# Performance work log

Measured on AMD Instinct MI355X. Metric: run time of the kernel, lower is better.

The kernel has to match this reference:

```python
import jax, jax.numpy as jnp
import numpy as np

B, C_IN, N, K, UP = 4, 128, 1024, 9, 4
EPS_BN = 1e-5


def _grid():
    # gen_grid(4): num_x=num_y=2, linspace(-0.2,0.2,2) -> (4,2)
    g = jnp.linspace(-0.2, 0.2, 2)
    x, y = jnp.meshgrid(g, g, indexing='ij')
    return jnp.stack([x, y], axis=-1).reshape(-1, 2)


def _knn(x, k, dilation):
    # x: (B,C,N). L2-normalize features, matrix pairwise dist, top-k, dilated select.
    nrm = jnp.sqrt(jnp.sum(x * x, axis=1, keepdims=True))
    xn = x / jnp.maximum(nrm, 1e-12)
    xt = xn.transpose(0, 2, 1)                      # (B,N,C)
    sq = jnp.sum(xt * xt, axis=-1)                  # (B,N)
    dist = sq[:, :, None] - 2.0 * jnp.einsum('bnc,bmc->bnm', xt, xt) + sq[:, None, :]
    _, idx = jax.lax.top_k(-dist, k * dilation)     # k*d nearest (incl. self)
    return idx[:, :, ::dilation]                    # (B,N,k)


def _bn(x, g, b, axes):
    # training-mode batchnorm over given axes, channel axis = 1
    m = jnp.mean(x, axis=axes, keepdims=True)
    v = jnp.mean((x - m) ** 2, axis=axes, keepdims=True)
    sh = [1] * x.ndim
    sh[1] = -1
    return (x - m) * jax.lax.rsqrt(v + EPS_BN) * g.reshape(sh) + b.reshape(sh)


def _edge_conv(x, k, dil, W, g, b):
    # DGCNN edge conv: gather neighbors, [x_i, x_j-x_i], 1x1 conv, BN, relu, max over k
    idx = _knn(x, k, dil)                                        # (B,N,k)
    x_j = jax.vmap(lambda xx, ii: xx[:, ii])(x, idx)             # (B,C,N,k)
    x_i = jnp.broadcast_to(x[..., None], x_j.shape)
    feat = jnp.concatenate([x_i, x_j - x_i], axis=1)             # (B,2C,N,k)
    out = jnp.einsum('oc,bcnk->bonk', W, feat)
    out = jax.nn.relu(_bn(out, g, b, (0, 2, 3)))
    return jnp.max(out, axis=-1)                                 # (B,Cout,N)


def _conv1d(x, W, b):
    return jnp.einsum('oc,bcn->bon', W, x) + b[None, :, None]


def _atten(x, Wf, bf, gf, bef, Wg, bg, gg, beg, Wh, bh, gh, beh, gamma):
    # attention_unit / RA_Layer1 math (C=130)
    f = jax.nn.relu(_bn(_conv1d(x, Wf, bf), gf, bef, (0, 2)))    # (B,C/4,M)
    g_ = jax.nn.relu(_bn(_conv1d(x, Wg, bg), gg, beg, (0, 2)))
    h = jax.nn.relu(_bn(_conv1d(x, Wh, bh), gh, beh, (0, 2)))    # (B,C,M)
    s = jnp.einsum('bcn,bcm->bnm', g_, f)                        # g^T @ f: (B,M,M)
    beta = jax.nn.softmax(s, axis=2)
    o = jnp.einsum('bcn,bnm->bcm', h, beta)                      # h @ beta
    return gamma * o + x


def _forward(inp, Wa, gna, bta, Wb, gnb, btb, Wf, bf, gf, bef, Wg, bg, gg, beg,
             Wh, bh, gh, beh, gamma, W1, b1, W2, b2):
    x1 = _edge_conv(inp, K, 1, Wa, gna, bta)                     # (B,256,N)
    x2 = _edge_conv(inp, K, 2, Wb, gnb, btb)                     # (B,256,N)
    x = jnp.concatenate([x1, x2], axis=1)                        # (B,512,N)
    net = x.transpose(0, 2, 1).reshape(B, N * UP, 128)           # (B,4N,128)
    grid = jnp.repeat(_grid(), N, axis=0)                        # (4N,2)
    grid = jnp.broadcast_to(grid[None], (B, N * UP, 2)).astype(net.dtype)
    net = jnp.concatenate([net, grid], axis=2).transpose(0, 2, 1)  # (B,130,4N)
    net = _atten(net, Wf, bf, gf, bef, Wg, bg, gg, beg, Wh, bh, gh, beh, gamma)
    net = jax.nn.relu(_conv1d(net, W1, b1))                      # 130->256
    net = jax.nn.relu(_conv1d(net, W2, b2))                      # 256->128
    return net                                                   # (B,128,4N)


def setup_inputs() -> dict:
    key = jax.random.key(0)
    ks = jax.random.split(key, 24)
    rn = lambda k, sh, s=0.05: jax.random.normal(k, sh, jnp.float32) * s
    d = {
        'inp': jax.random.normal(ks[0], (B, C_IN, N), jnp.float32),
        'Wa': rn(ks[1], (256, 256)), 'gna': 1.0 + rn(ks[2], (256,)), 'bta': rn(ks[3], (256,)),
        'Wb': rn(ks[4], (256, 256)), 'gnb': 1.0 + rn(ks[5], (256,)), 'btb': rn(ks[6], (256,)),
        'Wf': rn(ks[7], (32, 130)), 'bf': rn(ks[8], (32,)), 'gf': 1.0 + rn(ks[9], (32,)), 'bef': rn(ks[9], (32,)),
        'Wg': rn(ks[10], (32, 130)), 'bg': rn(ks[11], (32,)), 'gg': 1.0 + rn(ks[12], (32,)), 'beg': rn(ks[12], (32,)),
        'Wh': rn(ks[13], (130, 130)), 'bh': rn(ks[14], (130,)), 'gh': 1.0 + rn(ks[15], (130,)), 'beh': rn(ks[15], (130,)),
        'gamma': rn(ks[16], (), 1.0),
        'W1': rn(ks[17], (256, 130)), 'b1': rn(ks[18], (256,)),
        'W2': rn(ks[19], (128, 256)), 'b2': rn(ks[20], (128,)),
    }
    return d


def reference(inp, Wa, gna, bta, Wb, gnb, btb, Wf, bf, gf, bef, Wg, bg, gg, beg,
              Wh, bh, gh, beh, gamma, W1, b1, W2, b2):
    return _forward(inp, Wa, gna, bta, Wb, gnb, btb, Wf, bf, gf, bef, Wg, bg, gg, beg,
                    Wh, bh, gh, beh, gamma, W1, b1, W2, b2)
```

## Files before the change

### kernel.cpp

```cpp
#include <hip/hip_runtime.h>

namespace {
constexpr int NB = 4;
constexpr int CI = 128;
constexpr int NP = 1024;
constexpr int MM = 4096;
constexpr float EPSBN = 1e-5f;
constexpr float LOG2E = 1.4426950408889634f;

constexpr size_t OPS_SH = 2162688;
constexpr size_t OFF_OP   = 0;
constexpr size_t OFF_DIST = 0;
constexpr size_t OFF_PM   = 0;
constexpr size_t OFF_QM   = 2097152;
constexpr size_t OFF_HRAW = 0;
constexpr size_t OFF_FGRAW= 2359296;
constexpr size_t OFF_Y1   = 0;
constexpr size_t OFF_FGT  = 6488064;
constexpr size_t OFF_HB   = 7012352;
constexpr size_t OFF_A16  = 6488064;
constexpr size_t OFF_X16  = 8192000;
constexpr size_t OFF_LSE  = 9502720;
constexpr size_t OFF_LSEP = 9519104;
constexpr size_t OFF_STATS= 9650176;
constexpr size_t OFF_ABE  = 9715712;
constexpr size_t OFF_ABFG = 9716736;
constexpr size_t OFF_ABH  = 9716864;
constexpr size_t OFF_FGP  = 9717376;
constexpr size_t OFF_BIAS = 9725568;
constexpr size_t OFF_W16  = 9726208;
constexpr size_t OFF_KNN  = 9779712;
constexpr size_t OFF_XN   = 9853440;
constexpr size_t OFF_SQ   = 10377728;
constexpr size_t OFF_XR   = 10381824;
constexpr size_t OFF_WPQ  = 10643968;
constexpr size_t W16_FG = 0;
constexpr size_t W16_H  = 10240;
constexpr size_t W16_C1 = 33280;
constexpr size_t W16_C2 = 74240;
constexpr size_t B_FG = 0, B_H = 64, B_C1 = 208, B_C2 = 464;
}

typedef __attribute__((ext_vector_type(8))) short short8;
typedef __attribute__((ext_vector_type(4))) float f32x4;
#define MFMA16(A, B, C) __builtin_amdgcn_mfma_f32_16x16x32_bf16(A, B, C, 0, 0, 0)

__device__ inline unsigned short f2bf(float x) {
  unsigned int u = __float_as_uint(x);
  unsigned int r = u + 0x7fff + ((u >> 16) & 1);
  return (unsigned short)(r >> 16);
}
__device__ inline float bf2f(unsigned short s) {
  return __uint_as_float(((unsigned int)s) << 16);
}
__device__ inline unsigned cvtpk(float lo, float hi) {
  unsigned r;
  asm("v_cvt_pk_bf16_f32 %0, %1, %2" : "=v"(r) : "v"(lo), "v"(hi));
  return r;
}

__global__ __launch_bounds__(256) void k_prep(const float* __restrict__ Wf, const float* __restrict__ Wg,
                                              const float* __restrict__ Wh, const float* __restrict__ W1,
                                              const float* __restrict__ W2, const float* __restrict__ bf,
                                              const float* __restrict__ bg, const float* __restrict__ bh,
                                              const float* __restrict__ b1, const float* __restrict__ b2,
                                              unsigned short* __restrict__ W16, float* __restrict__ BIAS) {
  int i = blockIdx.x * 256 + threadIdx.x;
  if (i < 107008) {
    float v = 0.f;
    if (i < 10240) { int o = i / 160, c = i % 160; if (c < 130) v = (o < 32) ? Wf[o * 130 + c] : Wg[(o - 32) * 130 + c]; }
    else if (i < 33280) { int r = i - 10240; int o = r / 160, c = r % 160; if (o < 130 && c < 130) v = Wh[o * 130 + c]; }
    else if (i < 74240) { int r = i - 33280; int o = r / 160, c = r % 160; if (c < 130) v = W1[o * 130 + c]; }
    else { int r = i - 74240; int o = r / 256, c = r % 256; v = W2[o * 256 + c]; }
    W16[i] = f2bf(v);
  } else if (i < 107648) {
    int j = i - 107008; float v = 0.f;
    if (j < 64) v = (j < 32) ? bf[j] : bg[j - 32];
    else if (j < 208) { int c = j - 64; if (c < 130) v = bh[c]; }
    else if (j < 464) v = b1[j - 208];
    else if (j < 592) v = b2[j - 464];
    BIAS[j] = v;
  }
}

__global__ __launch_bounds__(256) void k_prep2(const float* __restrict__ Wa, const float* __restrict__ Wb,
                                               unsigned short* __restrict__ WPQ) {
  int i = blockIdx.x * 256 + threadIdx.x;
  int e = i >> 16;
  int rem = i & 65535;
  int pq = rem >> 15;
  int rr = rem & 32767;
  int o = rr >> 7, c = rr & 127;
  const float* W = e ? Wb : Wa;
  float w1 = W[o * 256 + c], w2 = W[o * 256 + 128 + c];
  float v = pq ? w2 : (w1 - w2);
  WPQ[i] = f2bf(v);
}

__global__ __launch_bounds__(256) void k_norm(const float* __restrict__ x,
                                              float* __restrict__ xn,
                                              unsigned short* __restrict__ XR,
                                              float* __restrict__ sq) {
  int t = blockIdx.x * 256 + threadIdx.x;
  int b = t >> 10, n = t & 1023;
  const float* xb = x + (size_t)b * CI * NP + n;
  float ss = 0.f;
  #pragma unroll 4
  for (int c = 0; c < CI; ++c) { float v = xb[(size_t)c * NP]; ss += v * v; }
  float inv = 1.f / fmaxf(sqrtf(ss), 1e-12f);
  float* xo = xn + (size_t)b * CI * NP + n;
  float s2 = 0.f;
  for (int c0 = 0; c0 < 128; c0 += 8) {
    unsigned rw[4];
    #pragma unroll
    for (int j = 0; j < 4; ++j) {
      float va = xb[(size_t)(c0 + 2 * j) * NP];
      float vb = xb[(size_t)(c0 + 2 * j + 1) * NP];
      float na = va * inv, nb = vb * inv;
      s2 += na * na + nb * nb;
      xo[(size_t)(c0 + 2 * j) * NP] = na;
      xo[(size_t)(c0 + 2 * j + 1) * NP] = nb;
      rw[j] = (unsigned)f2bf(va) | ((unsigned)f2bf(vb) << 16);
    }
    uint4 r4 = {rw[0], rw[1], rw[2], rw[3]};
    *(uint4*)&XR[(size_t)t * 128 + c0] = r4;
  }
  sq[t] = s2;
}

__global__ __launch_bounds__(256) void k_dist(const float* __restrict__ xn,
                                              const float* __restrict__ sq,
                                              float* __restrict__ dist) {
  __shared__ float As[32][68], Bs[32][68];
  int t = threadIdx.x;
  int m0 = blockIdx.x * 64, n0 = blockIdx.y * 64, b = blockIdx.z;
  int mg = t & 15, ng = t >> 4;
  float acc[16];
  #pragma unroll
  for (int i = 0; i < 16; ++i) acc[i] = 0.f;
  for (int cc = 0; cc < 128; cc += 32) {
    __syncthreads();
    for (int idx = t; idx < 2048; idx += 256) {
      int c = idx >> 6, j = idx & 63;
      As[c][j] = xn[((size_t)b * CI + cc + c) * NP + n0 + j];
      Bs[c][j] = xn[((size_t)b * CI + cc + c) * NP + m0 + j];
    }
    __syncthreads();
    #pragma unroll
    for (int c = 0; c < 32; ++c) {
      float4 avv = *(const float4*)&As[c][ng * 4];
      float4 bvv = *(const float4*)&Bs[c][mg * 4];
      float a[4] = {avv.x, avv.y, avv.z, avv.w};
      float bb[4] = {bvv.x, bvv.y, bvv.z, bvv.w};
      #pragma unroll
      for (int i = 0; i < 4; ++i)
        #pragma unroll
        for (int j = 0; j < 4; ++j) acc[i * 4 + j] += a[i] * bb[j];
    }
  }
  #pragma unroll
  for (int i = 0; i < 4; ++i) {
    int n = n0 + ng * 4 + i;
    float sn = sq[b * NP + n];
    float4 r;
    r.x = sn + sq[b * NP + m0 + mg * 4 + 0] - 2.f * acc[i * 4 + 0];
    r.y = sn + sq[b * NP + m0 + mg * 4 + 1] - 2.f * acc[i * 4 + 1];
    r.z = sn + sq[b * NP + m0 + mg * 4 + 2] - 2.f * acc[i * 4 + 2];
    r.w = sn + sq[b * NP + m0 + mg * 4 + 3] - 2.f * acc[i * 4 + 3];
    *(float4*)&dist[((size_t)b * NP + n) * NP + m0 + mg * 4] = r;
  }
}

__global__ __launch_bounds__(64) void k_knn(const float* __restrict__ dist,
                                            int* __restrict__ knn) {
  int row = blockIdx.x;
  int l = threadIdx.x;
  const float* dr = dist + (size_t)row * NP;
  float d[16];
  #pragma unroll
  for (int i = 0; i < 16; ++i) d[i] = dr[l + 64 * i];
  for (int s = 0; s < 18; ++s) {
    float best = __builtin_inff(); int bslot = -1;
    #pragma unroll
    for (int i = 0; i < 16; ++i) if (d[i] < best) { best = d[i]; bslot = i; }
    int bidx = (bslot >= 0) ? (l + 64 * bslot) : 0x7fffffff;
    float bd = best; int bi = bidx;
    #pragma unroll
    for (int off = 32; off > 0; off >>= 1) {
      float od = __shfl_xor(bd, off);
      int   oi = __shfl_xor(bi, off);
      if (od < bd || (od == bd && oi < bi)) { bd = od; bi = oi; }
    }
    if (l == 0) knn[row * 18 + s] = bi;
    if ((bi & 63) == l) d[bi >> 6] = __builtin_inff();
  }
}

__global__ __launch_bounds__(256) void k_pqm(const unsigned short* __restrict__ XR,
                                             const unsigned short* __restrict__ WPQ,
                                             float* __restrict__ Pm,
                                             float* __restrict__ Qm) {
  int t = threadIdx.x; int w = t >> 6; int l = t & 63;
  int lm = l & 15, g = l >> 4;
  int nt = blockIdx.x, oq = blockIdx.y, z = blockIdx.z;
  int e = z >> 2, b = z & 3;
  int srow = nt * 64 + w * 16 + lm;
  const unsigned short* sp = XR + ((size_t)b * 1024 + srow) * 128 + 8 * g;
  const unsigned short* wpp = WPQ + ((size_t)(e * 2 + 0) * 256 + oq * 64 + lm) * 128 + 8 * g;
  const unsigned short* wqq = WPQ + ((size_t)(e * 2 + 1) * 256 + oq * 64 + lm) * 128 + 8 * g;
  f32x4 accp[4], accq[4];
  #pragma unroll
  for (int i = 0; i < 4; ++i) { accp[i] = {0.f, 0.f, 0.f, 0.f}; accq[i] = {0.f, 0.f, 0.f, 0.f}; }
  #pragma unroll
  for (int cc = 0; cc < 4; ++cc) {
    short8 bfr = *(const short8*)(sp + cc * 32);
    #pragma unroll
    for (int ct = 0; ct < 4; ++ct) {
      short8 ap = *(const short8*)(wpp + (size_t)ct * 16 * 128 + cc * 32);
      accp[ct] = MFMA16(ap, bfr, accp[ct]);
      short8 aq = *(const short8*)(wqq + (size_t)ct * 16 * 128 + cc * 32);
      accq[ct] = MFMA16(aq, bfr, accq[ct]);
    }
  }
  int eb = e * 4 + b;
  #pragma unroll
  for (int ct = 0; ct < 4; ++ct) {
    int o0 = oq * 64 + ct * 16 + 4 * g;
    float4 rp = {accp[ct][0], accp[ct][1], accp[ct][2], accp[ct][3]};
    float4 rq = {accq[ct][0], accq[ct][1], accq[ct][2], accq[ct][3]};
    *(float4*)&Pm[((size_t)eb * 1024 + srow) * 256 + o0] = rp;
    *(float4*)&Qm[((size_t)eb * 1024 + srow) * 256 + o0] = rq;
  }
}

__global__ __launch_bounds__(256) void k_edge_stats(const float* __restrict__ Pm,
                                                    const float* __restrict__ Qm,
                                                    const int* __restrict__ knn,
                                                    float* __restrict__ stats) {
  int o = threadIdx.x;
  int chunk = blockIdx.x, b = blockIdx.y, e = blockIdx.z;
  int eb = e * 4 + b;
  float s = 0.f, s2 = 0.f;
  for (int nn = 0; nn < 64; ++nn) {
    int n = chunk * 64 + nn;
    float p = Pm[((size_t)eb * 1024 + n) * 256 + o];
    const int* kn = knn + (b * 1024 + n) * 18;
    #pragma unroll
    for (int kk = 0; kk < 9; ++kk) {
      int j = kn[e ? 2 * kk : kk];
      float v = p + Qm[((size_t)eb * 1024 + j) * 256 + o];
      s += v; s2 += v * v;
    }
  }
  size_t idx = ((((size_t)e * 4 + b) * 16 + chunk) * 256 + o) * 2;
  stats[idx] = s; stats[idx + 1] = s2;
}

__global__ __launch_bounds__(256) void k_edge_fin(const float* __restrict__ stats,
                                                  const float* __restrict__ gna, const float* __restrict__ bta,
                                                  const float* __restrict__ gnb, const float* __restrict__ btb,
                                                  float* __restrict__ ab) {
  int i = blockIdx.x * 256 + threadIdx.x;
  if (i >= 512) return;
  int e = i >> 8, o = i & 255;
  float s = 0.f, s2 = 0.f;
  for (int b = 0; b < 4; ++b)
    for (int ch = 0; ch < 16; ++ch) {
      size_t idx = ((((size_t)e * 4 + b) * 16 + ch) * 256 + o) * 2;
      s += stats[idx]; s2 += stats[idx + 1];
    }
  float cnt = 4.0f * 1024.0f * 9.0f;
  float mean = s / cnt;
  float var = s2 / cnt - mean * mean;
  float g = e ? gnb[o] : gna[o];
  float bt = e ? btb[o] : bta[o];
  float alpha = g * rsqrtf(var + EPSBN);
  ab[i * 2] = alpha; ab[i * 2 + 1] = bt - mean * alpha;
}

__global__ __launch_bounds__(256) void k_edge_apply(const float* __restrict__ Pm,
                                                    const float* __restrict__ Qm,
                                                    const int* __restrict__ knn,
                                                    const float* __restrict__ ab,
                                                    unsigned short* __restrict__ X16) {
  __shared__ int knl[18];
  int t = threadIdx.x;
  int n = blockIdx.x, b = blockIdx.y;
  if (t < 18) knl[t] = knn[(b * 1024 + n) * 18 + t];
  __syncthreads();
  int e = t >> 7, oo = t & 127;
  int eb = e * 4 + b;
  const float* Pr = Pm + ((size_t)eb * 1024 + n) * 256;
  const float* Qb = Qm + (size_t)eb * 1024 * 256;
  float p0 = Pr[oo], p1 = Pr[oo + 128];
  float a0 = ab[(e * 256 + oo) * 2], be0 = ab[(e * 256 + oo) * 2 + 1];
  float a1 = ab[(e * 256 + oo + 128) * 2], be1 = ab[(e * 256 + oo + 128) * 2 + 1];
  float mx0 = -__builtin_inff(), mx1 = -__builtin_inff();
  #pragma unroll
  for (int kk = 0; kk < 9; ++kk) {
    int j = knl[e ? 2 * kk : kk];
    const float* Qr = Qb + (size_t)j * 256;
    mx0 = fmaxf(mx0, fmaf(a0, p0 + Qr[oo], be0));
    mx1 = fmaxf(mx1, fmaf(a1, p1 + Qr[oo + 128], be1));
  }
  int u0 = e << 1, u1 = (e << 1) | 1;
  X16[((size_t)b * MM + 4 * n + u0) * 160 + oo] = f2bf(fmaxf(mx0, 0.f));
  X16[((size_t)b * MM + 4 * n + u1) * 160 + oo] = f2bf(fmaxf(mx1, 0.f));
  if (t < 128) {
    int u = t >> 5, c = 128 + (t & 31);
    int gr = n >> 8;
    float v = (c == 128) ? ((gr < 2) ? -0.2f : 0.2f) : (c == 129) ? ((gr & 1) ? 0.2f : -0.2f) : 0.f;
    X16[((size_t)b * MM + 4 * n + u) * 160 + c] = f2bf(v);
  }
}

template <int KSTEPS, int CTPER, int OUTMODE, bool RELU>
__global__ __launch_bounds__(256) void k_convm(const unsigned short* __restrict__ src,
                                               const unsigned short* __restrict__ W16,
                                               const float* __restrict__ bias,
                                               float* __restrict__ dstF,
                                               unsigned short* __restrict__ dstB,
                                               int outld, int rows) {
  constexpr int LD = KSTEPS * 32;
  int t = threadIdx.x; int w = t >> 6; int l = t & 63;
  int lm = l & 15, g = l >> 4;
  int b = blockIdx.z; int ct0 = blockIdx.y * CTPER;
  int srow = blockIdx.x * 64 + w * 16 + lm;
  const unsigned short* sp = src + ((size_t)b * MM + srow) * LD + 8 * g;
  const unsigned short* wp = W16 + ((size_t)ct0 * 16 + lm) * LD + 8 * g;
  f32x4 acc[CTPER];
  #pragma unroll
  for (int i = 0; i < CTPER; ++i) acc[i] = {0.f, 0.f, 0.f, 0.f};
  #pragma unroll
  for (int cc = 0; cc < KSTEPS; ++cc) {
    short8 bfr = *(const short8*)(sp + cc * 32);
    #pragma unroll
    for (int ct = 0; ct < CTPER; ++ct) {
      short8 af = *(const short8*)(wp + (size_t)ct * 16 * LD + cc * 32);
      acc[ct] = MFMA16(af, bfr, acc[ct]);
    }
  }
  #pragma unroll
  for (int ct = 0; ct < CTPER; ++ct) {
    int o0 = (ct0 + ct) * 16 + 4 * g;
    float4 bv = *(const float4*)&bias[o0];
    float v[4] = {acc[ct][0] + bv.x, acc[ct][1] + bv.y, acc[ct][2] + bv.z, acc[ct][3] + bv.w};
    if (RELU) { v[0] = fmaxf(v[0], 0.f); v[1] = fmaxf(v[1], 0.f); v[2] = fmaxf(v[2], 0.f); v[3] = fmaxf(v[3], 0.f); }
    if (OUTMODE == 0) {
      float4 r = {v[0], v[1], v[2], v[3]};
      *(float4*)&dstF[((size_t)b * MM + srow) * outld + o0] = r;
    } else if (OUTMODE == 1) {
      uint2 pk;
      pk.x = cvtpk(v[0], v[1]);
      pk.y = cvtpk(v[2], v[3]);
      *(uint2*)&dstB[((size_t)b * MM + srow) * outld + o0] = pk;
    } else {
      #pragma unroll
      for (int r = 0; r < 4; ++r)
        dstF[((size_t)b * rows + o0 + r) * MM + srow] = v[r];
    }
  }
}

__global__ __launch_bounds__(256) void k_fgstats(const float* __restrict__ FGraw,
                                                 float* __restrict__ FGP) {
  __shared__ float red[4][64][2];
  int t = threadIdx.x; int c = t & 63, rq = t >> 6;
  int blk = blockIdx.x;
  float s = 0.f, s2 = 0.f;
  for (int k = 0; k < 64; ++k) {
    int r = blk * 256 + rq + 4 * k;
    float v = FGraw[(size_t)r * 64 + c];
    s += v; s2 += v * v;
  }
  red[rq][c][0] = s; red[rq][c][1] = s2;
  __syncthreads();
  if (t < 64) {
    float a = 0.f, a2 = 0.f;
    #pragma unroll
    for (int q = 0; q < 4; ++q) { a += red[q][t][0]; a2 += red[q][t][1]; }
    FGP[((size_t)blk * 64 + t) * 2] = a; FGP[((size_t)blk * 64 + t) * 2 + 1] = a2;
  }
}

__global__ __launch_bounds__(64) void k_fgfin(const float* __restrict__ FGP,
                                              const float* __restrict__ gf, const float* __restrict__ bef,
                                              const float* __restrict__ gg, const float* __restrict__ beg,
                                              float* __restrict__ ab) {
  int c = threadIdx.x;
  float s = 0.f, s2 = 0.f;
  for (int blk = 0; blk < 64; ++blk) { s += FGP[((size_t)blk * 64 + c) * 2]; s2 += FGP[((size_t)blk * 64 + c) * 2 + 1]; }
  float cnt = 16384.f;
  float mean = s / cnt, var = s2 / cnt - mean * mean;
  float gv = (c < 32) ? gf[c] : gg[c - 32];
  float bv = (c < 32) ? bef[c] : beg[c - 32];
  float alpha = gv * rsqrtf(var + EPSBN);
  ab[c * 2] = alpha; ab[c * 2 + 1] = bv - mean * alpha;
}

__global__ __launch_bounds__(256) void k_bnstats(const float* __restrict__ src,
                                                 const float* __restrict__ g,
                                                 const float* __restrict__ be,
                                                 float* __restrict__ ab, int ldC) {
  int o = blockIdx.x;
  int t = threadIdx.x;
  float s = 0.f, s2 = 0.f;
  for (int b = 0; b < NB; ++b) {
    const float* r = src + ((size_t)b * ldC + o) * MM;
    for (int m = t; m < MM; m += 256) { float v = r[m]; s += v; s2 += v * v; }
  }
  __shared__ float rs[256], rs2[256];
  rs[t] = s; rs2[t] = s2;
  __syncthreads();
  for (int off = 128; off > 0; off >>= 1) {
    if (t < off) { rs[t] += rs[t + off]; rs2[t] += rs2[t + off]; }
    __syncthreads();
  }
  if (t == 0) {
    float cnt = 16384.0f;
    float mean = rs[0] / cnt, var = rs2[0] / cnt - mean * mean;
    float alpha = g[o] * rsqrtf(var + EPSBN);
    ab[o * 2] = alpha; ab[o * 2 + 1] = be[o] - mean * alpha;
  }
}

__global__ __launch_bounds__(256) void k_cvtFG(const float* __restrict__ FGraw,
                                               const float* __restrict__ ab,
                                               unsigned short* __restrict__ FGT) {
  int i = blockIdx.x * 256 + threadIdx.x;
  int row = i >> 3, c0 = (i & 7) * 8;
  float sc = (c0 < 32) ? LOG2E : 1.0f;
  float vv[8];
  float4 u0 = *(const float4*)&FGraw[(size_t)row * 64 + c0];
  float4 u1 = *(const float4*)&FGraw[(size_t)row * 64 + c0 + 4];
  vv[0] = u0.x; vv[1] = u0.y; vv[2] = u0.z; vv[3] = u0.w;
  vv[4] = u1.x; vv[5] = u1.y; vv[6] = u1.z; vv[7] = u1.w;
  uint4 pk;
  unsigned pw[4];
  #pragma unroll
  for (int h = 0; h < 4; ++h) {
    int c = c0 + 2 * h;
    float a0 = ab[c * 2] * sc, b0 = ab[c * 2 + 1] * sc;
    float a1 = ab[(c + 1) * 2] * sc, b1 = ab[(c + 1) * 2 + 1] * sc;
    float x0 = fmaxf(fmaf(a0, vv[2 * h], b0), 0.f);
    float x1 = fmaxf(fmaf(a1, vv[2 * h + 1], b1), 0.f);
    pw[h] = cvtpk(x0, x1);
  }
  pk.x = pw[0]; pk.y = pw[1]; pk.z = pw[2]; pk.w = pw[3];
  *(uint4*)&FGT[(size_t)row * 64 + c0] = pk;
}

__global__ __launch_bounds__(256) void k_cvtH(const float* __restrict__ src,
                                              const float* __restrict__ ab,
                                              unsigned short* __restrict__ dst) {
  int i = blockIdx.x * 256 + threadIdx.x;
  int m4 = i & 1023; int c = (i >> 10) % 144; int b = i / (144 * 1024);
  ushort4 ov = {0, 0, 0, 0};
  if (c < 130) {
    float4 v = *(const float4*)&src[((size_t)b * 144 + c) * MM + m4 * 4];
    float a = ab[c * 2], be = ab[c * 2 + 1];
    ov.x = f2bf(fmaxf(fmaf(a, v.x, be), 0.f));
    ov.y = f2bf(fmaxf(fmaf(a, v.y, be), 0.f));
    ov.z = f2bf(fmaxf(fmaf(a, v.z, be), 0.f));
    ov.w = f2bf(fmaxf(fmaf(a, v.w, be), 0.f));
  }
  *(ushort4*)&dst[((size_t)b * 144 + c) * MM + m4 * 4] = ov;
}

__global__ __launch_bounds__(256) void k_zlse(const unsigned short* __restrict__ FGT,
                                              float* __restrict__ LSEP) {
  int t = threadIdx.x; int w = t >> 6; int l = t & 63;
  int b = blockIdx.z; int ms = blockIdx.y;
  int n0 = blockIdx.x * 64 + w * 16;
  int lm = l & 15, g = l >> 4;
  f32x4 z4 = {0.f, 0.f, 0.f, 0.f};
  short8 af = *(const short8*)&FGT[((size_t)b * MM + n0 + lm) * 64 + 32 + 8 * g];
  float rm[4], zz[4];
  #pragma unroll
  for (int r = 0; r < 4; ++r) { rm[r] = -__builtin_inff(); zz[r] = 0.f; }
  for (int it = 0; it < 16; ++it) {
    int m0 = ms * 1024 + it * 64;
    short8 bfr[4];
    #pragma unroll
    for (int mi = 0; mi < 4; ++mi)
      bfr[mi] = *(const short8*)&FGT[((size_t)b * MM + m0 + mi * 16 + lm) * 64 + 8 * g];
    f32x4 d[4];
    #pragma unroll
    for (int mi = 0; mi < 4; ++mi) d[mi] = MFMA16(af, bfr[mi], z4);
    #pragma unroll
    for (int r = 0; r < 4; ++r) {
      float tm = fmaxf(fmaxf(d[0][r], d[1][r]), fmaxf(d[2][r], d[3][r]));
      float nm = fmaxf(rm[r], tm);
      zz[r] = zz[r] * exp2f(rm[r] - nm)
            + exp2f(d[0][r] - nm) + exp2f(d[1][r] - nm)
            + exp2f(d[2][r] - nm) + exp2f(d[3][r] - nm);
      rm[r] = nm;
    }
  }
  #pragma unroll
  for (int off = 1; off < 16; off <<= 1) {
    #pragma unroll
    for (int r = 0; r < 4; ++r) {
      float om = __shfl_xor(rm[r], off);
      float oz = __shfl_xor(zz[r], off);
      float nm = fmaxf(rm[r], om);
      zz[r] = zz[r] * exp2f(rm[r] - nm) + oz * exp2f(om - nm);
      rm[r] = nm;
    }
  }
  if (lm == 0) {
    #pragma unroll
    for (int r = 0; r < 4; ++r) {
      int n = n0 + 4 * g + r;
      size_t idx = ((size_t)ms * 16384 + (size_t)b * MM + n) * 2;
      LSEP[idx] = rm[r]; LSEP[idx + 1] = zz[r];
    }
  }
}

__global__ __launch_bounds__(256) void k_lsered(const float* __restrict__ LSEP,
                                                float* __restrict__ LSE) {
  int bn = blockIdx.x * 256 + threadIdx.x;
  float rm = -__builtin_inff(), zz = 0.f;
  #pragma unroll
  for (int ms = 0; ms < 4; ++ms) {
    float m = LSEP[((size_t)ms * 16384 + bn) * 2];
    float z = LSEP[((size_t)ms * 16384 + bn) * 2 + 1];
    float nm = fmaxf(rm, m);
    zz = zz * exp2f(rm - nm) + z * exp2f(m - nm);
    rm = nm;
  }
  LSE[bn] = rm + log2f(zz);
}

__global__ __launch_bounds__(256) void k_omfma(const unsigned short* __restrict__ FGT,
                                               const unsigned short* __restrict__ HB,
                                               const float* __restrict__ LSE,
                                               unsigned short* __restrict__ Opart) {
  int t = threadIdx.x; int w = t >> 6; int l = t & 63;
  int b = blockIdx.y; int split = blockIdx.z;
  int lm = l & 15, g = l >> 4;
  int mcol0 = blockIdx.x * 128 + w * 32 + lm;
  int mcol1 = mcol0 + 16;
  f32x4 z4 = {0.f, 0.f, 0.f, 0.f};
  short8 Ff0 = *(const short8*)&FGT[((size_t)b * MM + mcol0) * 64 + 8 * g];
  short8 Ff1 = *(const short8*)&FGT[((size_t)b * MM + mcol1) * 64 + 8 * g];
  f32x4 acc0[9], acc1[9];
  #pragma unroll
  for (int ct = 0; ct < 9; ++ct) { acc0[ct] = z4; acc1[ct] = z4; }
  const int nchunks = (split < 2) ? 22 : 21;
  const int startc = split * 21 + ((split < 2) ? split : 2);
  const int start = startc * 32;
  const int end = start + nchunks * 32;
  const unsigned short* gptr = FGT + ((size_t)b * MM + lm) * 64 + 32 + 8 * g;
  const unsigned short* hbase = HB + ((size_t)b * 144 + lm) * MM + 8 * g;
  const float* lbase = LSE + (size_t)b * MM + 4 * g;
  int src01 = lm + 16 * (2 * (g & 1));
  int src23 = src01 + 16;
  bool hi = g >= 2;

  short8 a0 = *(const short8*)(gptr + (size_t)start * 64);
  short8 a1 = *(const short8*)(gptr + (size_t)(start + 16) * 64);
  float4 l0 = *(const float4*)(lbase + start);
  float4 l1 = *(const float4*)(lbase + start + 16);

  for (int n0 = start; n0 < end; n0 += 32) {
    const unsigned short* hp = hbase + n0;
    short8 hf[9];
    #pragma unroll
    for (int ct = 0; ct < 9; ++ct) hf[ct] = *(const short8*)(hp + (size_t)ct * 16 * MM);
    f32x4 s00 = MFMA16(a0, Ff0, z4);
    f32x4 s10 = MFMA16(a1, Ff0, z4);
    f32x4 s01 = MFMA16(a0, Ff1, z4);
    f32x4 s11 = MFMA16(a1, Ff1, z4);
    int nn = (n0 + 32 < end) ? (n0 + 32) : start;
    short8 na0 = *(const short8*)(gptr + (size_t)nn * 64);
    short8 na1 = *(const short8*)(gptr + (size_t)(nn + 16) * 64);
    float4 nl0 = *(const float4*)(lbase + nn);
    float4 nl1 = *(const float4*)(lbase + nn + 16);
    float le0[4] = {l0.x, l0.y, l0.z, l0.w};
    float le1[4] = {l1.x, l1.y, l1.z, l1.w};
    unsigned pk00[2], pk10[2], pk01[2], pk11[2];
    #pragma unroll
    for (int h2 = 0; h2 < 2; ++h2) {
      float e00a = exp2f(s00[2 * h2] - le0[2 * h2]);
      float e00b = exp2f(s00[2 * h2 + 1] - le0[2 * h2 + 1]);
      float e10a = exp2f(s10[2 * h2] - le1[2 * h2]);
      float e10b = exp2f(s10[2 * h2 + 1] - le1[2 * h2 + 1]);
      float e01a = exp2f(s01[2 * h2] - le0[2 * h2]);
      float e01b = exp2f(s01[2 * h2 + 1] - le0[2 * h2 + 1]);
      float e11a = exp2f(s11[2 * h2] - le1[2 * h2]);
      float e11b = exp2f(s11[2 * h2 + 1] - le1[2 * h2 + 1]);
      pk00[h2] = cvtpk(e00a, e00b);
      pk10[h2] = cvtpk(e10a, e10b);
      pk01[h2] = cvtpk(e01a, e01b);
      pk11[h2] = cvtpk(e11a, e11b);
    }
    a0 = na0; a1 = na1; l0 = nl0; l1 = nl1;
    unsigned a0w = (unsigned)__shfl((int)pk00[0], src01);
    unsigned b0w = (unsigned)__shfl((int)pk10[0], src01);
    unsigned a1w = (unsigned)__shfl((int)pk00[1], src01);
    unsigned b1w = (unsigned)__shfl((int)pk10[1], src01);
    unsigned a2w = (unsigned)__shfl((int)pk00[0], src23);
    unsigned b2w = (unsigned)__shfl((int)pk10[0], src23);
    unsigned a3w = (unsigned)__shfl((int)pk00[1], src23);
    unsigned b3w = (unsigned)__shfl((int)pk10[1], src23);
    union { unsigned u[4]; short8 s; } bu0;
    bu0.u[0] = hi ? b0w : a0w; bu0.u[1] = hi ? b1w : a1w;
    bu0.u[2] = hi ? b2w : a2w; bu0.u[3] = hi ? b3w : a3w;
    short8 bfrag0 = bu0.s;
    unsigned c0w = (unsigned)__shfl((int)pk01[0], src01);
    unsigned d0w = (unsigned)__shfl((int)pk11[0], src01);
    unsigned c1w = (unsigned)__shfl((int)pk01[1], src01);
    unsigned d1w = (unsigned)__shfl((int)pk11[1], src01);
    unsigned c2w = (unsigned)__shfl((int)pk01[0], src23);
    unsigned d2w = (unsigned)__shfl((int)pk11[0], src23);
    unsigned c3w = (unsigned)__shfl((int)pk01[1], src23);
    unsigned d3w = (unsigned)__shfl((int)pk11[1], src23);
    union { unsigned u[4]; short8 s; } bu1;
    bu1.u[0] = hi ? d0w : c0w; bu1.u[1] = hi ? d1w : c1w;
    bu1.u[2] = hi ? d2w : c2w; bu1.u[3] = hi ? d3w : c3w;
    short8 bfrag1 = bu1.s;
    #pragma unroll
    for (int ct = 0; ct < 9; ++ct) {
      acc0[ct] = MFMA16(hf[ct], bfrag0, acc0[ct]);
      acc1[ct] = MFMA16(hf[ct], bfrag1, acc1[ct]);
    }
  }
  unsigned short* op0 = Opart + (size_t)split * OPS_SH + ((size_t)b * MM + mcol0) * 132;
  unsigned short* op1 = Opart + (size_t)split * OPS_SH + ((size_t)b * MM + mcol1) * 132;
  #pragma unroll
  for (int ct = 0; ct < 9; ++ct) {
    int c0 = ct * 16 + 4 * g;
    if (c0 < 132) {
      uint2 p0, p1;
      p0.x = cvtpk(acc0[ct][0], acc0[ct][1]);
      p0.y = cvtpk(acc0[ct][2], acc0[ct][3]);
      p1.x = cvtpk(acc1[ct][0], acc1[ct][1]);
      p1.y = cvtpk(acc1[ct][2], acc1[ct][3]);
      *(uint2*)&op0[c0] = p0;
      *(uint2*)&op1[c0] = p1;
    }
  }
}

__global__ __launch_bounds__(256) void k_ored(const unsigned short* __restrict__ Op,
                                              const unsigned short* __restrict__ X16,
                                              const float* __restrict__ gma,
                                              unsigned short* __restrict__ A16) {
  int i = blockIdx.x * 256 + threadIdx.x;
  int row = i / 20, c8 = i % 20;
  int c0 = c8 * 8;
  unsigned short* ap = A16 + (size_t)row * 160 + c0;
  if (c0 >= 136) {
    uint4 z = {0, 0, 0, 0};
    *(uint4*)ap = z;
    return;
  }
  float gm = gma[0];
  float ov[8] = {0.f, 0.f, 0.f, 0.f, 0.f, 0.f, 0.f, 0.f};
  #pragma unroll
  for (int s = 0; s < 6; ++s) {
    const unsigned short* base = Op + (size_t)s * OPS_SH + (size_t)row * 132 + c0;
    uint2 u = *(const uint2*)base;
    ov[0] += bf2f((unsigned short)(u.x & 0xffff));
    ov[1] += bf2f((unsigned short)(u.x >> 16));
    ov[2] += bf2f((unsigned short)(u.y & 0xffff));
    ov[3] += bf2f((unsigned short)(u.y >> 16));
    if (c0 + 4 < 132) {
      uint2 v = *(const uint2*)(base + 4);
      ov[4] += bf2f((unsigned short)(v.x & 0xffff));
      ov[5] += bf2f((unsigned short)(v.x >> 16));
      ov[6] += bf2f((unsigned short)(v.y & 0xffff));
      ov[7] += bf2f((unsigned short)(v.y >> 16));
    }
  }
  short8 xv = *(const short8*)(X16 + (size_t)row * 160 + c0);
  unsigned pw[4];
  #pragma unroll
  for (int h = 0; h < 4; ++h) {
    int ca = c0 + 2 * h, cb = c0 + 2 * h + 1;
    float xa = bf2f((unsigned short)xv[2 * h]);
    float xb = bf2f((unsigned short)xv[2 * h + 1]);
    float va = (ca < 132) ? (gm * ov[2 * h] + xa) : 0.f;
    float vb = (cb < 132) ? (gm * ov[2 * h + 1] + xb) : 0.f;
    pw[h] = (unsigned)f2bf(va) | ((unsigned)f2bf(vb) << 16);
  }
  uint4 pk = {pw[0], pw[1], pw[2], pw[3]};
  *(uint4*)ap = pk;
}

extern "C" void kernel_launch(void* const* d_in, const int* in_sizes, int n_in,
                              void* d_out, int out_size, void* d_ws, size_t ws_size,
                              hipStream_t stream) {
  const float* inp = (const float*)d_in[0];
  const float* Wa  = (const float*)d_in[1];
  const float* gna = (const float*)d_in[2];
  const float* bta = (const float*)d_in[3];
  const float* Wb  = (const float*)d_in[4];
  const float* gnb = (const float*)d_in[5];
  const float* btb = (const float*)d_in[6];
  const float* Wf  = (const float*)d_in[7];
  const float* bf  = (const float*)d_in[8];
  const float* gf  = (const float*)d_in[9];
  const float* bef = (const float*)d_in[10];
  const float* Wg  = (const float*)d_in[11];
  const float* bg  = (const float*)d_in[12];
  const float* gg  = (const float*)d_in[13];
  const float* beg = (const float*)d_in[14];
  const float* Wh  = (const float*)d_in[15];
  const float* bh  = (const float*)d_in[16];
  const float* gh  = (const float*)d_in[17];
  const float* beh = (const float*)d_in[18];
  const float* gamma = (const float*)d_in[19];
  const float* W1  = (const float*)d_in[20];
  const float* b1  = (const float*)d_in[21];
  const float* W2  = (const float*)d_in[22];
  const float* b2  = (const float*)d_in[23];
  float* out = (float*)d_out;

  float* ws = (float*)d_ws;
  float* DIST = ws + OFF_DIST;
  float* PM   = ws + OFF_PM;
  float* QM   = ws + OFF_QM;
  float* HRAW = ws + OFF_HRAW;
  float* FGRAW= ws + OFF_FGRAW;
  unsigned short* OP16 = (unsigned short*)(ws + OFF_OP);
  unsigned short* FGT = (unsigned short*)(ws + OFF_FGT);
  unsigned short* HBB = (unsigned short*)(ws + OFF_HB);
  unsigned short* A16 = (unsigned short*)(ws + OFF_A16);
  unsigned short* X16 = (unsigned short*)(ws + OFF_X16);
  unsigned short* Y1  = (unsigned short*)(ws + OFF_Y1);
  float* LSEB = ws + OFF_LSE;
  float* LSEP = ws + OFF_LSEP;
  float* STATS= ws + OFF_STATS;
  float* ABE  = ws + OFF_ABE;
  float* ABFG = ws + OFF_ABFG;
  float* ABH  = ws + OFF_ABH;
  float* FGP  = ws + OFF_FGP;
  float* BIAS = ws + OFF_BIAS;
  unsigned short* W16 = (unsigned short*)(ws + OFF_W16);
  int*   KNNI = (int*)(ws + OFF_KNN);
  float* XN   = ws + OFF_XN;
  unsigned short* XR = (unsigned short*)(ws + OFF_XR);
  unsigned short* WPQ = (unsigned short*)(ws + OFF_WPQ);
  float* SQ   = ws + OFF_SQ;

  k_prep<<<421, 256, 0, stream>>>(Wf, Wg, Wh, W1, W2, bf, bg, bh, b1, b2, W16, BIAS);
  k_prep2<<<512, 256, 0, stream>>>(Wa, Wb, WPQ);
  k_norm<<<16, 256, 0, stream>>>(inp, XN, XR, SQ);
  k_dist<<<dim3(16, 16, 4), 256, 0, stream>>>(XN, SQ, DIST);
  k_knn<<<4096, 64, 0, stream>>>(DIST, KNNI);
  k_pqm<<<dim3(16, 4, 8), 256, 0, stream>>>(XR, WPQ, PM, QM);
  k_edge_stats<<<dim3(16, 4, 2), 256, 0, stream>>>(PM, QM, KNNI, STATS);
  k_edge_fin<<<2, 256, 0, stream>>>(STATS, gna, bta, gnb, btb, ABE);
  k_edge_apply<<<dim3(1024, 4), 256, 0, stream>>>(PM, QM, KNNI, ABE, X16);
  k_convm<5, 2, 0, false><<<dim3(64, 2, 4), 256, 0, stream>>>(X16, W16 + W16_FG, BIAS + B_FG, FGRAW, nullptr, 64, 0);
  k_convm<5, 3, 2, false><<<dim3(64, 3, 4), 256, 0, stream>>>(X16, W16 + W16_H, BIAS + B_H, HRAW, nullptr, 0, 144);
  k_fgstats<<<64, 256, 0, stream>>>(FGRAW, FGP);
  k_fgfin<<<1, 64, 0, stream>>>(FGP, gf, bef, gg, beg, ABFG);
  k_bnstats<<<130, 256, 0, stream>>>(HRAW, gh, beh, ABH, 144);
  k_cvtFG<<<512, 256, 0, stream>>>(FGRAW, ABFG, FGT);
  k_cvtH<<<2304, 256, 0, stream>>>(HRAW, ABH, HBB);
  k_zlse<<<dim3(64, 4, 4), 256, 0, stream>>>(FGT, LSEP);
  k_lsered<<<64, 256, 0, stream>>>(LSEP, LSEB);
  k_omfma<<<dim3(32, 4, 6), 256, 0, stream>>>(FGT, HBB, LSEB, OP16);
  k_ored<<<1280, 256, 0, stream>>>(OP16, X16, gamma, A16);
  k_convm<5, 8, 1, true><<<dim3(64, 2, 4), 256, 0, stream>>>(A16, W16 + W16_C1, BIAS + B_C1, nullptr, Y1, 256, 0);
  k_convm<8, 4, 2, true><<<dim3(64, 2, 4), 256, 0, stream>>>(Y1, W16 + W16_C2, BIAS + B_C2, out, nullptr, 0, 128);
}
```

Baseline: 352.3 us.

## Stage H tiles through double-buffered LDS in omfma and merge prep kernels

```diff
diff --git a/kernel.cpp b/kernel.cpp
--- a/kernel.cpp
+++ b/kernel.cpp
@@ -64,7 +64,9 @@
                                               const float* __restrict__ W2, const float* __restrict__ bf,
                                               const float* __restrict__ bg, const float* __restrict__ bh,
                                               const float* __restrict__ b1, const float* __restrict__ b2,
-                                              unsigned short* __restrict__ W16, float* __restrict__ BIAS) {
+                                              const float* __restrict__ Wa, const float* __restrict__ Wb,
+                                              unsigned short* __restrict__ W16, float* __restrict__ BIAS,
+                                              unsigned short* __restrict__ WPQ) {
   int i = blockIdx.x * 256 + threadIdx.x;
   if (i < 107008) {
     float v = 0.f;
@@ -80,21 +82,18 @@
     else if (j < 464) v = b1[j - 208];
     else if (j < 592) v = b2[j - 464];
     BIAS[j] = v;
-  }
-}
-
-__global__ __launch_bounds__(256) void k_prep2(const float* __restrict__ Wa, const float* __restrict__ Wb,
-                                               unsigned short* __restrict__ WPQ) {
-  int i = blockIdx.x * 256 + threadIdx.x;
-  int e = i >> 16;
-  int rem = i & 65535;
-  int pq = rem >> 15;
-  int rr = rem & 32767;
-  int o = rr >> 7, c = rr & 127;
-  const float* W = e ? Wb : Wa;
-  float w1 = W[o * 256 + c], w2 = W[o * 256 + 128 + c];
-  float v = pq ? w2 : (w1 - w2);
-  WPQ[i] = f2bf(v);
+  } else if (i < 238720) {
+    int j = i - 107648;
+    int e = j >> 16;
+    int rem = j & 65535;
+    int pq = rem >> 15;
+    int rr = rem & 32767;
+    int o = rr >> 7, c = rr & 127;
+    const float* W = e ? Wb : Wa;
+    float w1 = W[o * 256 + c], w2 = W[o * 256 + 128 + c];
+    float v = pq ? w2 : (w1 - w2);
+    WPQ[j] = f2bf(v);
+  }
 }
 
 __global__ __launch_bounds__(256) void k_norm(const float* __restrict__ x,
@@ -537,6 +536,7 @@
                                                const unsigned short* __restrict__ HB,
                                                const float* __restrict__ LSE,
                                                unsigned short* __restrict__ Opart) {
+  __shared__ __align__(16) unsigned short Hs[2][144 * 40];
   int t = threadIdx.x; int w = t >> 6; int l = t & 63;
   int b = blockIdx.y; int split = blockIdx.z;
   int lm = l & 15, g = l >> 4;
@@ -551,52 +551,66 @@
   const int nchunks = (split < 2) ? 22 : 21;
   const int startc = split * 21 + ((split < 2) ? split : 2);
   const int start = startc * 32;
-  const int end = start + nchunks * 32;
   const unsigned short* gptr = FGT + ((size_t)b * MM + lm) * 64 + 32 + 8 * g;
-  const unsigned short* hbase = HB + ((size_t)b * 144 + lm) * MM + 8 * g;
+  const unsigned short* hsrc = HB + (size_t)b * 144 * MM;
   const float* lbase = LSE + (size_t)b * MM + 4 * g;
   int src01 = lm + 16 * (2 * (g & 1));
   int src23 = src01 + 16;
   bool hi = g >= 2;
-
+  int sidx0 = t, sidx1 = t + 256, sidx2 = t + 512;
+  int ch0 = sidx0 >> 2, sg0 = sidx0 & 3;
+  int ch1 = sidx1 >> 2, sg1 = sidx1 & 3;
+  int ch2 = (sidx2 < 576) ? (sidx2 >> 2) : 0;
+  int sg2 = sidx2 & 3;
+  bool has2 = sidx2 < 576;
+
+  {
+    uint4 r0 = *(const uint4*)(hsrc + (size_t)ch0 * MM + start + sg0 * 8);
+    uint4 r1 = *(const uint4*)(hsrc + (size_t)ch1 * MM + start + sg1 * 8);
+    uint4 r2 = has2 ? *(const uint4*)(hsrc + (size_t)ch2 * MM + start + sg2 * 8) : uint4{0,0,0,0};
+    *(uint4*)&Hs[0][ch0 * 40 + sg0 * 8] = r0;
+    *(uint4*)&Hs[0][ch1 * 40 + sg1 * 8] = r1;
+    if (has2) *(uint4*)&Hs[0][ch2 * 40 + sg2 * 8] = r2;
+  }
   short8 a0 = *(const short8*)(gptr + (size_t)start * 64);
   short8 a1 = *(const short8*)(gptr + (size_t)(start + 16) * 64);
   float4 l0 = *(const float4*)(lbase + start);
   float4 l1 = *(const float4*)(lbase + start + 16);
-
-  for (int n0 = start; n0 < end; n0 += 32) {
-    const unsigned short* hp = hbase + n0;
+  __syncthreads();
+
+  for (int it = 0; it < nchunks; ++it) {
+    int n0 = start + it * 32;
+    int cur = it & 1;
+    bool more = (it + 1 < nchunks);
+    int n1 = more ? (n0 + 32) : start;
+    uint4 r0, r1, r2;
+    if (more) {
+      r0 = *(const uint4*)(hsrc + (size_t)ch0 * MM + n1 + sg0 * 8);
+      r1 = *(const uint4*)(hsrc + (size_t)ch1 * MM + n1 + sg1 * 8);
+      if (has2) r2 = *(const uint4*)(hsrc + (size_t)ch2 * MM + n1 + sg2 * 8);
+    }
+    short8 na0 = *(const short8*)(gptr + (size_t)n1 * 64);
+    short8 na1 = *(const short8*)(gptr + (size_t)(n1 + 16) * 64);
+    float4 nl0 = *(const float4*)(lbase + n1);
+    float4 nl1 = *(const float4*)(lbase + n1 + 16);
     short8 hf[9];
     #pragma unroll
-    for (int ct = 0; ct < 9; ++ct) hf[ct] = *(const short8*)(hp + (size_t)ct * 16 * MM);
+    for (int ct = 0; ct < 9; ++ct)
+      hf[ct] = *(const short8*)&Hs[cur][(lm + 16 * ct) * 40 + g * 8];
     f32x4 s00 = MFMA16(a0, Ff0, z4);
     f32x4 s10 = MFMA16(a1, Ff0, z4);
     f32x4 s01 = MFMA16(a0, Ff1, z4);
     f32x4 s11 = MFMA16(a1, Ff1, z4);
-    int nn = (n0 + 32 < end) ? (n0 + 32) : start;
-    short8 na0 = *(const short8*)(gptr + (size_t)nn * 64);
-    short8 na1 = *(const short8*)(gptr + (size_t)(nn + 16) * 64);
-    float4 nl0 = *(const float4*)(lbase + nn);
-    float4 nl1 = *(const float4*)(lbase + nn + 16);
     float le0[4] = {l0.x, l0.y, l0.z, l0.w};
     float le1[4] = {l1.x, l1.y, l1.z, l1.w};
     unsigned pk00[2], pk10[2], pk01[2], pk11[2];
     #pragma unroll
     for (int h2 = 0; h2 < 2; ++h2) {
-      float e00a = exp2f(s00[2 * h2] - le0[2 * h2]);
-      float e00b = exp2f(s00[2 * h2 + 1] - le0[2 * h2 + 1]);
-      float e10a = exp2f(s10[2 * h2] - le1[2 * h2]);
-      float e10b = exp2f(s10[2 * h2 + 1] - le1[2 * h2 + 1]);
-      float e01a = exp2f(s01[2 * h2] - le0[2 * h2]);
-      float e01b = exp2f(s01[2 * h2 + 1] - le0[2 * h2 + 1]);
-      float e11a = exp2f(s11[2 * h2] - le1[2 * h2]);
-      float e11b = exp2f(s11[2 * h2 + 1] - le1[2 * h2 + 1]);
-      pk00[h2] = cvtpk(e00a, e00b);
-      pk10[h2] = cvtpk(e10a, e10b);
-      pk01[h2] = cvtpk(e01a, e01b);
-      pk11[h2] = cvtpk(e11a, e11b);
-    }
-    a0 = na0; a1 = na1; l0 = nl0; l1 = nl1;
+      pk00[h2] = cvtpk(exp2f(s00[2*h2] - le0[2*h2]), exp2f(s00[2*h2+1] - le0[2*h2+1]));
+      pk10[h2] = cvtpk(exp2f(s10[2*h2] - le1[2*h2]), exp2f(s10[2*h2+1] - le1[2*h2+1]));
+      pk01[h2] = cvtpk(exp2f(s01[2*h2] - le0[2*h2]), exp2f(s01[2*h2+1] - le0[2*h2+1]));
+      pk11[h2] = cvtpk(exp2f(s11[2*h2] - le1[2*h2]), exp2f(s11[2*h2+1] - le1[2*h2+1]));
+    }
     unsigned a0w = (unsigned)__shfl((int)pk00[0], src01);
     unsigned b0w = (unsigned)__shfl((int)pk10[0], src01);
     unsigned a1w = (unsigned)__shfl((int)pk00[1], src01);
@@ -621,12 +635,22 @@
     bu1.u[0] = hi ? d0w : c0w; bu1.u[1] = hi ? d1w : c1w;
     bu1.u[2] = hi ? d2w : c2w; bu1.u[3] = hi ? d3w : c3w;
     short8 bfrag1 = bu1.s;
+    __builtin_amdgcn_s_setprio(1);
     #pragma unroll
     for (int ct = 0; ct < 9; ++ct) {
       acc0[ct] = MFMA16(hf[ct], bfrag0, acc0[ct]);
       acc1[ct] = MFMA16(hf[ct], bfrag1, acc1[ct]);
     }
-  }
+    __builtin_amdgcn_s_setprio(0);
+    if (more) {
+      *(uint4*)&Hs[cur ^ 1][ch0 * 40 + sg0 * 8] = r0;
+      *(uint4*)&Hs[cur ^ 1][ch1 * 40 + sg1 * 8] = r1;
+      if (has2) *(uint4*)&Hs[cur ^ 1][ch2 * 40 + sg2 * 8] = r2;
+    }
+    a0 = na0; a1 = na1; l0 = nl0; l1 = nl1;
+    __syncthreads();
+  }
+
   unsigned short* op0 = Opart + (size_t)split * OPS_SH + ((size_t)b * MM + mcol0) * 132;
   unsigned short* op1 = Opart + (size_t)split * OPS_SH + ((size_t)b * MM + mcol1) * 132;
   #pragma unroll
@@ -746,8 +770,7 @@
   unsigned short* WPQ = (unsigned short*)(ws + OFF_WPQ);
   float* SQ   = ws + OFF_SQ;
 
-  k_prep<<<421, 256, 0, stream>>>(Wf, Wg, Wh, W1, W2, bf, bg, bh, b1, b2, W16, BIAS);
-  k_prep2<<<512, 256, 0, stream>>>(Wa, Wb, WPQ);
+  k_prep<<<933, 256, 0, stream>>>(Wf, Wg, Wh, W1, W2, bf, bg, bh, b1, b2, Wa, Wb, W16, BIAS, WPQ);
   k_norm<<<16, 256, 0, stream>>>(inp, XN, XR, SQ);
   k_dist<<<dim3(16, 16, 4), 256, 0, stream>>>(XN, SQ, DIST);
   k_knn<<<4096, 64, 0, stream>>>(DIST, KNNI);
```

New measurement: 316.0 us. 1.11x faster.
